# Kernel optimization log

Measured on AMD Instinct MI355X. Metric: run time of the kernel, lower is better.

The kernel has to match this reference:

```python
import jax, jax.numpy as jnp
import numpy as np

N = 20000   # nodes
E = 640000  # edges (avg degree 32)
D = 128     # input_nf == output_nf
H = 128     # hidden_size


def silu(x):
    return x * jax.nn.sigmoid(x)


def setup_inputs() -> dict:
    key = jax.random.key(0)
    ks = jax.random.split(key, 16)
    def lin(k, out_d, in_d, scale=None):
        s = scale if scale is not None else (1.0 / np.sqrt(in_d))
        return jax.random.uniform(k, (out_d, in_d), jnp.float32, -s, s)
    return {
        "h": jax.random.normal(ks[0], (N, D), jnp.float32),
        "coord": jax.random.normal(ks[1], (N, 3), jnp.float32),
        "edge_index": jax.random.randint(ks[2], (2, E), 0, N, jnp.int32),
        # edge_mlp: Linear(2D+1 -> H), Linear(H -> H)
        "We1": lin(ks[3], H, 2 * D + 1), "be1": jnp.zeros((H,), jnp.float32),
        "We2": lin(ks[4], H, H),          "be2": jnp.zeros((H,), jnp.float32),
        # node_mlp: Linear(H+D -> H), Linear(H -> D)
        "Wn1": lin(ks[5], H, H + D),      "bn1": jnp.zeros((H,), jnp.float32),
        "Wn2": lin(ks[6], D, H),          "bn2": jnp.zeros((D,), jnp.float32),
        # coord_mlp: Linear(H -> H), Linear(H -> 1, no bias, xavier gain=0.001)
        "Wc1": lin(ks[7], H, H),          "bc1": jnp.zeros((H,), jnp.float32),
        "Wc2": lin(ks[8], 1, H, scale=0.001 * np.sqrt(6.0 / (H + 1))),
    }


def reference(h, coord, edge_index, We1, be1, We2, be2, Wn1, bn1, Wn2, bn2, Wc1, bc1, Wc2):
    src, dst = edge_index[0], edge_index[1]

    # coord2radial (normalize=False)
    coord_diff = coord[src] - coord[dst]                 # [E, 3]
    radial = jnp.sum(coord_diff * coord_diff, axis=1, keepdims=True)  # [E, 1]

    # edge model: cat(h[src], h[dst], radial) -> Lin -> SiLU -> Lin -> SiLU
    e_in = jnp.concatenate([h[src], h[dst], radial], axis=1)  # [E, 2D+1]
    edge_feat = silu(silu(e_in @ We1.T + be1) @ We2.T + be2)  # [E, H]

    # coord model: coord_diff * coord_mlp(edge_feat), scatter-add over src
    w = silu(edge_feat @ Wc1.T + bc1) @ Wc2.T                 # [E, 1]
    trans = coord_diff * w                                    # [E, 3]
    coord_out = coord + jax.ops.segment_sum(trans, src, num_segments=N)

    # node model: agg edge_feat over src, cat(h, agg) -> Lin -> SiLU -> Lin, residual
    agg = jax.ops.segment_sum(edge_feat, src, num_segments=N)  # [N, H]
    n_in = jnp.concatenate([h, agg], axis=1)                   # [N, H+D]
    h_out = h + (silu(n_in @ Wn1.T + bn1) @ Wn2.T + bn2)       # [N, D]

    return (h_out, coord_out)
```

## Files before the change

### kernel.cpp

```cpp
#include <hip/hip_runtime.h>

#define N_NODES 20000
#define N_EDGES 640000
#define D 128
#define H 128

#define EB    128
#define TPB   512
#define NBLK2 512
#define NTILE (N_EDGES / EB)
#define EBN   64
#define NNT64 ((N_NODES + EBN - 1) / EBN)
#define NSCAT ((N_EDGES + 255) / 256)
#define ST    136

#define WS_W1   0
#define WS_W2   65536
#define WS_WC1  98304
#define WS_WN1  131072
#define WS_WN2  196608
#define WS_CNT  229376
#define WS_CUR  309376
#define WS_PERM 389376
#define WS_U    2949376
#define WS_V    8069376
#define WS_P    13189376

typedef short bf16x8 __attribute__((ext_vector_type(8)));
typedef float f32x4  __attribute__((ext_vector_type(4)));

__device__ __forceinline__ float silu_f(float x) {
    return x * __builtin_amdgcn_rcpf(1.0f + __expf(-x));
}
__device__ __forceinline__ ushort f2b(float f) {
    union { float f; unsigned int u; } v; v.f = f;
    return (ushort)((v.u + 0x7FFF + ((v.u >> 16) & 1)) >> 16);
}
__device__ __forceinline__ float b2f(ushort s) {
    union { unsigned int u; float f; } v; v.u = ((unsigned int)s) << 16; return v.f;
}
__device__ __forceinline__ unsigned f2b2(float lo, float hi) {
    unsigned r;
    asm("v_cvt_pk_bf16_f32 %0, %1, %2" : "=v"(r) : "v"(lo), "v"(hi));
    return r;
}

__device__ __forceinline__ void bar_lds() {
    asm volatile("s_waitcnt lgkmcnt(0)" ::: "memory");
    __builtin_amdgcn_s_barrier();
    asm volatile("" ::: "memory");
}

__device__ __forceinline__ void gemm_chunk_rw(const ushort* Ab, int kc0,
                                              const bf16x8 b[2], f32x4 acc[4][2],
                                              int eg, int lane)
{
    const int r = lane & 15, g = lane >> 4;
    bf16x8 a[4];
    #pragma unroll
    for (int mt = 0; mt < 4; ++mt)
        a[mt] = *(const bf16x8*)&Ab[(eg * 64 + mt * 16 + r) * ST + kc0 + g * 8];
    #pragma unroll
    for (int mt = 0; mt < 4; ++mt)
        #pragma unroll
        for (int nt = 0; nt < 2; ++nt)
            acc[mt][nt] = __builtin_amdgcn_mfma_f32_16x16x32_bf16(a[mt], b[nt], acc[mt][nt], 0, 0, 0);
}

__device__ __forceinline__ void zero_acc8(f32x4 acc[4][2]) {
    #pragma unroll
    for (int mt = 0; mt < 4; ++mt)
        #pragma unroll
        for (int nt = 0; nt < 2; ++nt)
            acc[mt][nt] = (f32x4){0.f, 0.f, 0.f, 0.f};
}

__device__ __forceinline__ void epi_silu8(f32x4 acc[4][2], const float* bias,
                                          ushort* out, int eg, int cg, int lane) {
    const int r = lane & 15, g = lane >> 4;
    #pragma unroll
    for (int nt = 0; nt < 2; ++nt) {
        int o = cg * 32 + nt * 16 + r;
        float bo = bias[o];
        #pragma unroll
        for (int mt = 0; mt < 4; ++mt)
            #pragma unroll
            for (int j = 0; j < 4; ++j) {
                int e = eg * 64 + mt * 16 + g * 4 + j;
                out[e * ST + o] = f2b(silu_f(acc[mt][nt][j] + bo));
            }
    }
}

__device__ __forceinline__ void epi_silu8_pk(f32x4 acc[4][2], const float* bias,
                                             ushort* out, int eg, int cg, int lane) {
    const int r = lane & 15, g = lane >> 4;
    #pragma unroll
    for (int nt = 0; nt < 2; ++nt) {
        int o = cg * 32 + nt * 16 + r;
        float bo = bias[o];
        #pragma unroll
        for (int mt = 0; mt < 4; ++mt) {
            int e = eg * 64 + mt * 16 + g * 4;
            unsigned p01 = f2b2(silu_f(acc[mt][nt][0] + bo), silu_f(acc[mt][nt][1] + bo));
            unsigned p23 = f2b2(silu_f(acc[mt][nt][2] + bo), silu_f(acc[mt][nt][3] + bo));
            out[(e + 0) * ST + o] = (ushort)p01;
            out[(e + 1) * ST + o] = (ushort)(p01 >> 16);
            out[(e + 2) * ST + o] = (ushort)p23;
            out[(e + 3) * ST + o] = (ushort)(p23 >> 16);
        }
    }
}

__global__ void prep2(const float* __restrict__ We1, const float* __restrict__ We2,
                      const float* __restrict__ Wc1, const float* __restrict__ Wn1,
                      const float* __restrict__ Wn2, const float* __restrict__ coordp,
                      const int* __restrict__ eidx,
                      ushort* w1, ushort* w2, ushort* wc1, ushort* wn1, ushort* wn2,
                      float* cout, int* cnt)
{
    int idx = blockIdx.x * 256 + threadIdx.x;
    if (idx < N_EDGES) atomicAdd(&cnt[eidx[idx]], 1);
    int j = idx;
    if (j < 32768) { w1[j] = f2b(We1[(j >> 8) * 257 + (j & 255)]); return; }
    j -= 32768;
    if (j < 16384) { w2[j] = f2b(We2[j]); return; }
    j -= 16384;
    if (j < 16384) { wc1[j] = f2b(Wc1[j]); return; }
    j -= 16384;
    if (j < 32768) { wn1[j] = f2b(Wn1[j]); return; }
    j -= 32768;
    if (j < 16384) { wn2[j] = f2b(Wn2[j]); return; }
    j -= 16384;
    if (j < N_NODES * 3) cout[j] = coordp[j];
}

__global__ void scan_k(const int* __restrict__ cnt, int* cur) {
    __shared__ int wsum[16];
    __shared__ int carry_s;
    const int t = threadIdx.x, lane = t & 63, wid = t >> 6;
    if (t == 0) carry_s = 0;
    __syncthreads();
    for (int base = 0; base < N_NODES; base += 1024) {
        int i = base + t;
        int vv = (i < N_NODES) ? cnt[i] : 0;
        int s = vv;
        #pragma unroll
        for (int d = 1; d < 64; d <<= 1) {
            int x = __shfl_up(s, d);
            if (lane >= d) s += x;
        }
        if (lane == 63) wsum[wid] = s;
        __syncthreads();
        if (wid == 0) {
            int ws = (lane < 16) ? wsum[lane] : 0;
            #pragma unroll
            for (int d = 1; d < 16; d <<= 1) {
                int x = __shfl_up(ws, d);
                if (lane >= d) ws += x;
            }
            if (lane < 16) wsum[lane] = ws;
        }
        __syncthreads();
        int woff = (wid > 0) ? wsum[wid - 1] : 0;
        if (i < N_NODES) cur[i] = carry_s + woff + s - vv;
        __syncthreads();
        if (t == 0) carry_s += wsum[15];
        __syncthreads();
    }
}

__global__ __launch_bounds__(256, 2)
void uvp_scatter_k(const float* __restrict__ h,
                   const ushort* __restrict__ w1b, const ushort* __restrict__ wn1b,
                   const float* __restrict__ be1, const float* __restrict__ bn1,
                   ushort* __restrict__ u, ushort* __restrict__ v, ushort* __restrict__ p,
                   const int* __restrict__ eidx, int* cur, int* perm)
{
    const int tid = threadIdx.x;
    if (blockIdx.x >= NNT64) {
        int e = (blockIdx.x - NNT64) * 256 + tid;
        if (e < N_EDGES) {
            int pp = atomicAdd(&cur[eidx[e]], 1);
            perm[pp] = e;
        }
        return;
    }
    __shared__ __align__(16) ushort hs[EBN * ST];
    __shared__ float b1s[H], bn1s[H];

    const int lane = tid & 63, wv = tid >> 6;
    const int eg = wv >> 2, cg = wv & 3;
    const int r = lane & 15, g = lane >> 4;
    const int n0 = blockIdx.x * EBN;

    if (tid < 128) b1s[tid] = be1[tid];
    else if (tid < 256) bn1s[tid - 128] = bn1[tid - 128];

    bf16x8 wa[4][2], wb[4][2], wn[4][2];
    {
        const int c0 = cg * 32 + r, c1c = c0 + 16;
        #pragma unroll
        for (int kc = 0; kc < 4; ++kc) {
            wa[kc][0] = *(const bf16x8*)&w1b [c0  * 256 +       kc * 32 + g * 8];
            wa[kc][1] = *(const bf16x8*)&w1b [c1c * 256 +       kc * 32 + g * 8];
            wb[kc][0] = *(const bf16x8*)&w1b [c0  * 256 + 128 + kc * 32 + g * 8];
            wb[kc][1] = *(const bf16x8*)&w1b [c1c * 256 + 128 + kc * 32 + g * 8];
            wn[kc][0] = *(const bf16x8*)&wn1b[c0  * 256 +       kc * 32 + g * 8];
            wn[kc][1] = *(const bf16x8*)&wn1b[c1c * 256 +       kc * 32 + g * 8];
        }
    }
    #pragma unroll
    for (int it = 0; it < 8; ++it) {
        int idx = tid + it * 256;
        int e = idx >> 5, c = idx & 31;
        int n = n0 + e; if (n >= N_NODES) n = 0;
        float4 vv = *(const float4*)&h[(size_t)n * D + c * 4];
        ushort4 pk; pk.x = f2b(vv.x); pk.y = f2b(vv.y); pk.z = f2b(vv.z); pk.w = f2b(vv.w);
        *(ushort4*)&hs[e * ST + c * 4] = pk;
    }
    __syncthreads();

    f32x4 acc[4][2];
    zero_acc8(acc);
    #pragma unroll
    for (int kc = 0; kc < 4; ++kc) gemm_chunk_rw(hs, kc * 32, wa[kc], acc, eg, lane);
    #pragma unroll
    for (int nt = 0; nt < 2; ++nt) {
        int o = cg * 32 + nt * 16 + r;
        float bo = b1s[o];
        #pragma unroll
        for (int mt = 0; mt < 4; ++mt)
            #pragma unroll
            for (int j = 0; j < 4; ++j) {
                int n = n0 + eg * 64 + mt * 16 + g * 4 + j;
                if (n < N_NODES) u[(size_t)n * H + o] = f2b(acc[mt][nt][j] + bo);
            }
    }
    zero_acc8(acc);
    #pragma unroll
    for (int kc = 0; kc < 4; ++kc) gemm_chunk_rw(hs, kc * 32, wb[kc], acc, eg, lane);
    #pragma unroll
    for (int nt = 0; nt < 2; ++nt) {
        int o = cg * 32 + nt * 16 + r;
        #pragma unroll
        for (int mt = 0; mt < 4; ++mt)
            #pragma unroll
            for (int j = 0; j < 4; ++j) {
                int n = n0 + eg * 64 + mt * 16 + g * 4 + j;
                if (n < N_NODES) v[(size_t)n * H + o] = f2b(acc[mt][nt][j]);
            }
    }
    zero_acc8(acc);
    #pragma unroll
    for (int kc = 0; kc < 4; ++kc) gemm_chunk_rw(hs, kc * 32, wn[kc], acc, eg, lane);
    #pragma unroll
    for (int nt = 0; nt < 2; ++nt) {
        int o = cg * 32 + nt * 16 + r;
        float bo = bn1s[o];
        #pragma unroll
        for (int mt = 0; mt < 4; ++mt)
            #pragma unroll
            for (int j = 0; j < 4; ++j) {
                int n = n0 + eg * 64 + mt * 16 + g * 4 + j;
                if (n < N_NODES) p[(size_t)n * H + o] = f2b(acc[mt][nt][j] + bo);
            }
    }
}

__global__ __launch_bounds__(TPB, 2)
void egcl_edge(const ushort* __restrict__ u, const ushort* __restrict__ v,
               const int* __restrict__ eidx, const int* __restrict__ perm,
               const float* __restrict__ coordp,
               const ushort* __restrict__ w2b, const ushort* __restrict__ wc1b,
               const float* __restrict__ We1,
               const float* __restrict__ be2, const float* __restrict__ bc1,
               const float* __restrict__ Wc2,
               float* __restrict__ agg, float* __restrict__ coord_out)
{
    __shared__ __align__(16) ushort t1[EB * ST];
    __shared__ __align__(16) ushort ef[EB * ST];
    __shared__ int   srcs_s[2][EB], dsts_s[2][EB];
    __shared__ float radial_s[2][EB];
    __shared__ float cdx_s[2][EB], cdy_s[2][EB], cdz_s[2][EB];
    __shared__ float wcop[4][EB];
    __shared__ float b2s[H], bc1s[H], wc2s[H], w256s[H];

    const int tid = threadIdx.x, lane = tid & 63, wv = tid >> 6;
    const int eg = wv >> 2, cg = wv & 3;
    const int r = lane & 15, g = lane >> 4;
    const int ce = tid >> 2, cq = tid & 3;

    if (tid < 128)      b2s[tid] = be2[tid];
    else if (tid < 256) bc1s[tid - 128] = bc1[tid - 128];
    else if (tid < 384) wc2s[tid - 256] = Wc2[tid - 256];
    else                w256s[tid - 384] = We1[(tid - 384) * 257 + 256];

    bf16x8 w2f[4][2], w3f[4][2];
    {
        const int c0 = cg * 32 + r, c1c = c0 + 16;
        #pragma unroll
        for (int kc = 0; kc < 4; ++kc) {
            w2f[kc][0] = *(const bf16x8*)&w2b [c0  * 128 + kc * 32 + g * 8];
            w2f[kc][1] = *(const bf16x8*)&w2b [c1c * 128 + kc * 32 + g * 8];
            w3f[kc][0] = *(const bf16x8*)&wc1b[c0  * 128 + kc * 32 + g * 8];
            w3f[kc][1] = *(const bf16x8*)&wc1b[c1c * 128 + kc * 32 + g * 8];
        }
    }

    int t = (int)blockIdx.x;
    int rs = 0, rd = 0;
    float rsx = 0, rsy = 0, rsz = 0, rdx = 0, rdy = 0, rdz = 0;
    if (tid < EB) {
        int e = perm[t * EB + tid];
        int s = eidx[e], d = eidx[N_EDGES + e];
        srcs_s[0][tid] = s; dsts_s[0][tid] = d;
        float sx = coordp[s * 3], sy = coordp[s * 3 + 1], sz = coordp[s * 3 + 2];
        float dx0 = coordp[d * 3], dy0 = coordp[d * 3 + 1], dz0 = coordp[d * 3 + 2];
        float dx = sx - dx0, dy = sy - dy0, dz = sz - dz0;
        cdx_s[0][tid] = dx; cdy_s[0][tid] = dy; cdz_s[0][tid] = dz;
        radial_s[0][tid] = dx * dx + dy * dy + dz * dz;
    }
    __syncthreads();

    bf16x8 uvr[8];
    {
        const ushort* up = u + (size_t)srcs_s[0][ce] * H + cq * 32;
        const ushort* vp = v + (size_t)dsts_s[0][ce] * H + cq * 32;
        #pragma unroll
        for (int i = 0; i < 4; ++i) {
            uvr[i]     = *(const bf16x8*)(up + i * 8);
            uvr[4 + i] = *(const bf16x8*)(vp + i * 8);
        }
    }
    if (tid < EB && t + NBLK2 < NTILE) {
        int e = perm[(t + NBLK2) * EB + tid];
        rs = eidx[e]; rd = eidx[N_EDGES + e];
        rsx = coordp[rs * 3]; rsy = coordp[rs * 3 + 1]; rsz = coordp[rs * 3 + 2];
        rdx = coordp[rd * 3]; rdy = coordp[rd * 3 + 1]; rdz = coordp[rd * 3 + 2];
    }

    f32x4 acc[4][2];
    int pb = 0;

    for (; t < NTILE; t += NBLK2) {
        {
            float rad = radial_s[pb][ce];
            #pragma unroll
            for (int i = 0; i < 4; ++i) {
                float4 wlo = *(const float4*)&w256s[cq * 32 + i * 8];
                float4 whi = *(const float4*)&w256s[cq * 32 + i * 8 + 4];
                bf16x8 uu = uvr[i], vx = uvr[4 + i];
                float x0 = silu_f(b2f((ushort)uu[0]) + b2f((ushort)vx[0]) + rad * wlo.x);
                float x1 = silu_f(b2f((ushort)uu[1]) + b2f((ushort)vx[1]) + rad * wlo.y);
                float x2 = silu_f(b2f((ushort)uu[2]) + b2f((ushort)vx[2]) + rad * wlo.z);
                float x3 = silu_f(b2f((ushort)uu[3]) + b2f((ushort)vx[3]) + rad * wlo.w);
                float x4 = silu_f(b2f((ushort)uu[4]) + b2f((ushort)vx[4]) + rad * whi.x);
                float x5 = silu_f(b2f((ushort)uu[5]) + b2f((ushort)vx[5]) + rad * whi.y);
                float x6 = silu_f(b2f((ushort)uu[6]) + b2f((ushort)vx[6]) + rad * whi.z);
                float x7 = silu_f(b2f((ushort)uu[7]) + b2f((ushort)vx[7]) + rad * whi.w);
                uint4 pk4;
                pk4.x = f2b2(x0, x1); pk4.y = f2b2(x2, x3);
                pk4.z = f2b2(x4, x5); pk4.w = f2b2(x6, x7);
                *(uint4*)&t1[ce * ST + cq * 32 + i * 8] = pk4;
            }
        }
        if (tid < EB) {
            srcs_s[pb ^ 1][tid] = rs; dsts_s[pb ^ 1][tid] = rd;
            float dx = rsx - rdx, dy = rsy - rdy, dz = rsz - rdz;
            cdx_s[pb ^ 1][tid] = dx; cdy_s[pb ^ 1][tid] = dy; cdz_s[pb ^ 1][tid] = dz;
            radial_s[pb ^ 1][tid] = dx * dx + dy * dy + dz * dz;
        }
        bar_lds();

        int en = 0;
        if (tid < EB && t + 2 * NBLK2 < NTILE) en = perm[(t + 2 * NBLK2) * EB + tid];
        zero_acc8(acc);
        __builtin_amdgcn_s_setprio(1);
        #pragma unroll
        for (int kc = 0; kc < 4; ++kc) gemm_chunk_rw(t1, kc * 32, w2f[kc], acc, eg, lane);
        __builtin_amdgcn_s_setprio(0);
        epi_silu8_pk(acc, b2s, ef, eg, cg, lane);
        bar_lds();

        {
            const ushort* up = u + (size_t)srcs_s[pb ^ 1][ce] * H + cq * 32;
            const ushort* vp = v + (size_t)dsts_s[pb ^ 1][ce] * H + cq * 32;
            #pragma unroll
            for (int i = 0; i < 4; ++i) {
                uvr[i]     = *(const bf16x8*)(up + i * 8);
                uvr[4 + i] = *(const bf16x8*)(vp + i * 8);
            }
        }
        int rs2 = 0, rd2 = 0;
        if (tid < EB) { rs2 = eidx[en]; rd2 = eidx[N_EDGES + en]; }
        {
            f32x4 acc3[2][4];
            #pragma unroll
            for (int ot = 0; ot < 2; ++ot)
                #pragma unroll
                for (int et = 0; et < 4; ++et)
                    acc3[ot][et] = (f32x4){0.f, 0.f, 0.f, 0.f};
            __builtin_amdgcn_s_setprio(1);
            #pragma unroll
            for (int kc = 0; kc < 4; ++kc) {
                bf16x8 bfr[4];
                #pragma unroll
                for (int et = 0; et < 4; ++et)
                    bfr[et] = *(const bf16x8*)&ef[(eg * 64 + et * 16 + r) * ST + kc * 32 + g * 8];
                #pragma unroll
                for (int ot = 0; ot < 2; ++ot)
                    #pragma unroll
                    for (int et = 0; et < 4; ++et)
                        acc3[ot][et] = __builtin_amdgcn_mfma_f32_16x16x32_bf16(
                            w3f[kc][ot], bfr[et], acc3[ot][et], 0, 0, 0);
            }
            __builtin_amdgcn_s_setprio(0);
            float partial[4] = {0.f, 0.f, 0.f, 0.f};
            #pragma unroll
            for (int ot = 0; ot < 2; ++ot) {
                int ob = cg * 32 + ot * 16 + g * 4;
                float4 wq = *(const float4*)&wc2s[ob];
                float4 bq = *(const float4*)&bc1s[ob];
                #pragma unroll
                for (int et = 0; et < 4; ++et) {
                    partial[et] += silu_f(acc3[ot][et][0] + bq.x) * wq.x
                                 + silu_f(acc3[ot][et][1] + bq.y) * wq.y
                                 + silu_f(acc3[ot][et][2] + bq.z) * wq.z
                                 + silu_f(acc3[ot][et][3] + bq.w) * wq.w;
                }
            }
            #pragma unroll
            for (int et = 0; et < 4; ++et) {
                float s_ = partial[et];
                s_ += __shfl_xor(s_, 16);
                s_ += __shfl_xor(s_, 32);
                if (g == 0) wcop[cg][eg * 64 + et * 16 + r] = s_;
            }
        }
        {
            int o = tid & 127, q = tid >> 7;
            int base = q * 32;
            float sum = 0.f;
            int curs = srcs_s[pb][base];
            for (int k = 0; k < 32; ++k) {
                int e = base + k;
                int s = srcs_s[pb][e];
                if (s != curs) {
                    atomicAdd(&agg[(size_t)curs * D + o], sum);
                    sum = 0.f; curs = s;
                }
                sum += b2f(ef[e * ST + o]);
            }
            atomicAdd(&agg[(size_t)curs * D + o], sum);
        }
        bar_lds();

        if (tid < EB) {
            rs = rs2; rd = rd2;
            rsx = coordp[rs * 3]; rsy = coordp[rs * 3 + 1]; rsz = coordp[rs * 3 + 2];
            rdx = coordp[rd * 3]; rdy = coordp[rd * 3 + 1]; rdz = coordp[rd * 3 + 2];
        }
        {
            float s_ = wcop[cq][ce];
            s_ += __shfl_down(s_, 2);
            s_ += __shfl_down(s_, 1);
            float wfull = __shfl(s_, lane & ~3);
            if (cq < 3) {
                float cdv = (cq == 0) ? cdx_s[pb][ce] : (cq == 1) ? cdy_s[pb][ce] : cdz_s[pb][ce];
                atomicAdd(&coord_out[(size_t)srcs_s[pb][ce] * 3 + cq], cdv * wfull);
            }
        }
        bar_lds();
        pb ^= 1;
    }
}

__global__ __launch_bounds__(256, 4)
void egcl_node(const float* __restrict__ h,
               const ushort* __restrict__ wn1b, const ushort* __restrict__ wn2b,
               const ushort* __restrict__ pArr, const float* __restrict__ bn2,
               float* __restrict__ hout )
{
    __shared__ __align__(16) ushort t1[EBN * ST];
    __shared__ __align__(16) ushort t2[EBN * ST];
    __shared__ float b2s[H];

    const int tid = threadIdx.x, lane = tid & 63, wv = tid >> 6;
    const int eg = wv >> 2, cg = wv & 3;
    const int r = lane & 15, g = lane >> 4;
    const int n0 = blockIdx.x * EBN;

    if (tid < 128) b2s[tid] = bn2[tid];

    bf16x8 wnb[4][2], w2f[4][2];
    {
        const int c0 = cg * 32 + r, c1c = c0 + 16;
        #pragma unroll
        for (int kc = 0; kc < 4; ++kc) {
            wnb[kc][0] = *(const bf16x8*)&wn1b[c0  * 256 + 128 + kc * 32 + g * 8];
            wnb[kc][1] = *(const bf16x8*)&wn1b[c1c * 256 + 128 + kc * 32 + g * 8];
            w2f[kc][0] = *(const bf16x8*)&wn2b[c0  * 128 + kc * 32 + g * 8];
            w2f[kc][1] = *(const bf16x8*)&wn2b[c1c * 128 + kc * 32 + g * 8];
        }
    }
    #pragma unroll
    for (int it = 0; it < 8; ++it) {
        int idx = tid + it * 256;
        int e = idx >> 5, c = idx & 31;
        int n = n0 + e; if (n >= N_NODES) n = 0;
        float4 vv = *(const float4*)&hout[(size_t)n * D + c * 4];
        ushort4 pk; pk.x = f2b(vv.x); pk.y = f2b(vv.y); pk.z = f2b(vv.z); pk.w = f2b(vv.w);
        *(ushort4*)&t1[e * ST + c * 4] = pk;
    }
    __syncthreads();

    f32x4 acc[4][2];
    zero_acc8(acc);
    #pragma unroll
    for (int kc = 0; kc < 4; ++kc) gemm_chunk_rw(t1, kc * 32, wnb[kc], acc, eg, lane);
    #pragma unroll
    for (int nt = 0; nt < 2; ++nt) {
        int o = cg * 32 + nt * 16 + r;
        #pragma unroll
        for (int mt = 0; mt < 4; ++mt)
            #pragma unroll
            for (int j = 0; j < 4; ++j) {
                int e = eg * 64 + mt * 16 + g * 4 + j;
                int n = n0 + e; if (n >= N_NODES) n = 0;
                float x = acc[mt][nt][j] + b2f(pArr[(size_t)n * H + o]);
                t2[e * ST + o] = f2b(silu_f(x));
            }
    }
    __syncthreads();

    zero_acc8(acc);
    #pragma unroll
    for (int kc = 0; kc < 4; ++kc) gemm_chunk_rw(t2, kc * 32, w2f[kc], acc, eg, lane);
    #pragma unroll
    for (int nt = 0; nt < 2; ++nt) {
        int o = cg * 32 + nt * 16 + r;
        float bo = b2s[o];
        #pragma unroll
        for (int mt = 0; mt < 4; ++mt)
            #pragma unroll
            for (int j = 0; j < 4; ++j) {
                int n = n0 + eg * 64 + mt * 16 + g * 4 + j;
                if (n < N_NODES)
                    hout[(size_t)n * D + o] = h[(size_t)n * D + o] + acc[mt][nt][j] + bo;
            }
    }
}

extern "C" void kernel_launch(void* const* d_in, const int* in_sizes, int n_in,
                              void* d_out, int out_size, void* d_ws, size_t ws_size,
                              hipStream_t stream)
{
    const float* h     = (const float*)d_in[0];
    const float* coord = (const float*)d_in[1];
    const int*   eidx  = (const int*)d_in[2];
    const float* We1 = (const float*)d_in[3];
    const float* be1 = (const float*)d_in[4];
    const float* We2 = (const float*)d_in[5];
    const float* be2 = (const float*)d_in[6];
    const float* Wn1 = (const float*)d_in[7];
    const float* bn1 = (const float*)d_in[8];
    const float* Wn2 = (const float*)d_in[9];
    const float* bn2 = (const float*)d_in[10];
    const float* Wc1 = (const float*)d_in[11];
    const float* bc1 = (const float*)d_in[12];
    const float* Wc2 = (const float*)d_in[13];

    float* hout = (float*)d_out;
    float* cout = (float*)d_out + (size_t)N_NODES * D;

    char* ws = (char*)d_ws;
    ushort* w1b  = (ushort*)(ws + WS_W1);
    ushort* w2b  = (ushort*)(ws + WS_W2);
    ushort* wc1b = (ushort*)(ws + WS_WC1);
    ushort* wn1b = (ushort*)(ws + WS_WN1);
    ushort* wn2b = (ushort*)(ws + WS_WN2);
    int* cnt  = (int*)(ws + WS_CNT);
    int* cur  = (int*)(ws + WS_CUR);
    int* perm = (int*)(ws + WS_PERM);
    ushort* uArr = (ushort*)(ws + WS_U);
    ushort* vArr = (ushort*)(ws + WS_V);
    ushort* pArr = (ushort*)(ws + WS_P);

    hipMemsetAsync(hout, 0, (size_t)N_NODES * D * sizeof(float), stream);
    hipMemsetAsync(cnt, 0, N_NODES * sizeof(int), stream);
    prep2<<<(N_EDGES + 255) / 256, 256, 0, stream>>>(We1, We2, Wc1, Wn1, Wn2, coord, eidx,
                                                     w1b, w2b, wc1b, wn1b, wn2b, cout, cnt);
    scan_k<<<1, 1024, 0, stream>>>(cnt, cur);
    uvp_scatter_k<<<NNT64 + NSCAT, 256, 0, stream>>>(
        h, w1b, wn1b, be1, bn1, uArr, vArr, pArr, eidx, cur, perm);
    egcl_edge<<<NBLK2, TPB, 0, stream>>>(uArr, vArr, eidx, perm, coord,
                                         w2b, wc1b, We1, be2, bc1, Wc2,
                                         hout, cout);
    egcl_node<<<NNT64, 256, 0, stream>>>(h, wn1b, wn2b, pArr, bn2, hout);
}
```

Measured before the change: 320.5 us.

## Defer coord scatter to next iteration to drop a barrier; fuse hout zeroing into prep

```diff
diff --git a/kernel.cpp b/kernel.cpp
--- a/kernel.cpp
+++ b/kernel.cpp
@@ -75,23 +75,6 @@
             acc[mt][nt] = (f32x4){0.f, 0.f, 0.f, 0.f};
 }
 
-__device__ __forceinline__ void epi_silu8(f32x4 acc[4][2], const float* bias,
-                                          ushort* out, int eg, int cg, int lane) {
-    const int r = lane & 15, g = lane >> 4;
-    #pragma unroll
-    for (int nt = 0; nt < 2; ++nt) {
-        int o = cg * 32 + nt * 16 + r;
-        float bo = bias[o];
-        #pragma unroll
-        for (int mt = 0; mt < 4; ++mt)
-            #pragma unroll
-            for (int j = 0; j < 4; ++j) {
-                int e = eg * 64 + mt * 16 + g * 4 + j;
-                out[e * ST + o] = f2b(silu_f(acc[mt][nt][j] + bo));
-            }
-    }
-}
-
 __device__ __forceinline__ void epi_silu8_pk(f32x4 acc[4][2], const float* bias,
                                              ushort* out, int eg, int cg, int lane) {
     const int r = lane & 15, g = lane >> 4;
@@ -117,10 +100,13 @@
                       const float* __restrict__ Wn2, const float* __restrict__ coordp,
                       const int* __restrict__ eidx,
                       ushort* w1, ushort* w2, ushort* wc1, ushort* wn1, ushort* wn2,
-                      float* cout, int* cnt)
+                      float* cout, int* cnt, float* hout)
 {
     int idx = blockIdx.x * 256 + threadIdx.x;
-    if (idx < N_EDGES) atomicAdd(&cnt[eidx[idx]], 1);
+    if (idx < N_EDGES) {
+        *(float4*)&hout[(size_t)idx * 4] = (float4){0.f, 0.f, 0.f, 0.f};
+        atomicAdd(&cnt[eidx[idx]], 1);
+    }
     int j = idx;
     if (j < 32768) { w1[j] = f2b(We1[(j >> 8) * 257 + (j & 255)]); return; }
     j -= 32768;
@@ -295,6 +281,7 @@
     else if (tid < 256) bc1s[tid - 128] = bc1[tid - 128];
     else if (tid < 384) wc2s[tid - 256] = Wc2[tid - 256];
     else                w256s[tid - 384] = We1[(tid - 384) * 257 + 256];
+    wcop[tid >> 7][tid & 127] = 0.f;
 
     bf16x8 w2f[4][2], w3f[4][2];
     {
@@ -342,8 +329,22 @@
 
     f32x4 acc[4][2];
     int pb = 0;
+    int fsrc = 0; float fcd = 0.f;
+    bool first = true;
 
     for (; t < NTILE; t += NBLK2) {
+        {
+            float s_ = wcop[cq][ce];
+            s_ += __shfl_down(s_, 2);
+            s_ += __shfl_down(s_, 1);
+            float wfull = __shfl(s_, lane & ~3);
+            if (cq < 3)
+                atomicAdd(&coord_out[(size_t)fsrc * 3 + cq], fcd * wfull);
+        }
+        if (!first && tid < EB) {
+            rsx = coordp[rs * 3]; rsy = coordp[rs * 3 + 1]; rsz = coordp[rs * 3 + 2];
+            rdx = coordp[rd * 3]; rdy = coordp[rd * 3 + 1]; rdz = coordp[rd * 3 + 2];
+        }
         {
             float rad = radial_s[pb][ce];
             #pragma unroll
@@ -365,16 +366,17 @@
                 *(uint4*)&t1[ce * ST + cq * 32 + i * 8] = pk4;
             }
         }
+        first = false;
+        bar_lds();
+
+        int en = 0;
+        if (tid < EB && t + 2 * NBLK2 < NTILE) en = perm[(t + 2 * NBLK2) * EB + tid];
         if (tid < EB) {
             srcs_s[pb ^ 1][tid] = rs; dsts_s[pb ^ 1][tid] = rd;
             float dx = rsx - rdx, dy = rsy - rdy, dz = rsz - rdz;
             cdx_s[pb ^ 1][tid] = dx; cdy_s[pb ^ 1][tid] = dy; cdz_s[pb ^ 1][tid] = dz;
             radial_s[pb ^ 1][tid] = dx * dx + dy * dy + dz * dz;
         }
-        bar_lds();
-
-        int en = 0;
-        if (tid < EB && t + 2 * NBLK2 < NTILE) en = perm[(t + 2 * NBLK2) * EB + tid];
         zero_acc8(acc);
         __builtin_amdgcn_s_setprio(1);
         #pragma unroll
@@ -438,6 +440,9 @@
                 if (g == 0) wcop[cg][eg * 64 + et * 16 + r] = s_;
             }
         }
+        fsrc = srcs_s[pb][ce];
+        fcd  = (cq == 0) ? cdx_s[pb][ce] : (cq == 1) ? cdy_s[pb][ce]
+             : (cq == 2) ? cdz_s[pb][ce] : 0.f;
         {
             int o = tid & 127, q = tid >> 7;
             int base = q * 32;
@@ -455,24 +460,17 @@
             atomicAdd(&agg[(size_t)curs * D + o], sum);
         }
         bar_lds();
-
-        if (tid < EB) {
-            rs = rs2; rd = rd2;
-            rsx = coordp[rs * 3]; rsy = coordp[rs * 3 + 1]; rsz = coordp[rs * 3 + 2];
-            rdx = coordp[rd * 3]; rdy = coordp[rd * 3 + 1]; rdz = coordp[rd * 3 + 2];
-        }
-        {
-            float s_ = wcop[cq][ce];
-            s_ += __shfl_down(s_, 2);
-            s_ += __shfl_down(s_, 1);
-            float wfull = __shfl(s_, lane & ~3);
-            if (cq < 3) {
-                float cdv = (cq == 0) ? cdx_s[pb][ce] : (cq == 1) ? cdy_s[pb][ce] : cdz_s[pb][ce];
-                atomicAdd(&coord_out[(size_t)srcs_s[pb][ce] * 3 + cq], cdv * wfull);
-            }
-        }
-        bar_lds();
+        rs = rs2; rd = rd2;
         pb ^= 1;
+    }
+
+    {
+        float s_ = wcop[cq][ce];
+        s_ += __shfl_down(s_, 2);
+        s_ += __shfl_down(s_, 1);
+        float wfull = __shfl(s_, lane & ~3);
+        if (cq < 3)
+            atomicAdd(&coord_out[(size_t)fsrc * 3 + cq], fcd * wfull);
     }
 }
 
@@ -587,10 +585,9 @@
     ushort* vArr = (ushort*)(ws + WS_V);
     ushort* pArr = (ushort*)(ws + WS_P);
 
-    hipMemsetAsync(hout, 0, (size_t)N_NODES * D * sizeof(float), stream);
     hipMemsetAsync(cnt, 0, N_NODES * sizeof(int), stream);
     prep2<<<(N_EDGES + 255) / 256, 256, 0, stream>>>(We1, We2, Wc1, Wn1, Wn2, coord, eidx,
-                                                     w1b, w2b, wc1b, wn1b, wn2b, cout, cnt);
+                                                     w1b, w2b, wc1b, wn1b, wn2b, cout, cnt, hout);
     scan_k<<<1, 1024, 0, stream>>>(cnt, cur);
     uvp_scatter_k<<<NNT64 + NSCAT, 256, 0, stream>>>(
         h, w1b, wn1b, be1, bn1, uArr, vArr, pArr, eidx, cur, perm);
```

Measured after the change: 1.069 ms. +233.6%, slower.
